# Performance work log

Measured on AMD Instinct MI355X. Metric: run time of the kernel, lower is better.

The kernel has to match this reference:

```python
import jax, jax.numpy as jnp
import numpy as np

N, E = 40000, 640000
IN_DIM, EDGE_DIM, HID = 128, 64, 128


def setup_inputs() -> dict:
    key = jax.random.key(0)
    ks = jax.random.split(key, 10)
    x = jax.random.normal(ks[0], (N, IN_DIM), dtype=jnp.float32)
    edge_index = jax.random.randint(ks[1], (2, E), 0, N, dtype=jnp.int64)
    edge_attr = jax.random.normal(ks[2], (E, EDGE_DIM), dtype=jnp.float32)
    # learned params (xavier-ish scaling)
    Wh_w = jax.random.normal(ks[3], (EDGE_DIM, HID), dtype=jnp.float32) / np.sqrt(EDGE_DIM)
    Wh_b = jnp.zeros((HID,), dtype=jnp.float32)
    Wn_w = jax.random.normal(ks[4], (2 * IN_DIM, HID), dtype=jnp.float32) / np.sqrt(2 * IN_DIM)
    Wn_b = jnp.zeros((HID,), dtype=jnp.float32)
    w_e = jax.random.normal(ks[5], (HID, 1), dtype=jnp.float32) / np.sqrt(HID)
    ft_w = jax.random.normal(ks[6], (IN_DIM, IN_DIM), dtype=jnp.float32) / np.sqrt(IN_DIM)
    ft_b = jnp.zeros((IN_DIM,), dtype=jnp.float32)
    return {"x": x, "edge_index": edge_index, "edge_attr": edge_attr,
            "Wh_w": Wh_w, "Wh_b": Wh_b, "Wn_w": Wn_w, "Wn_b": Wn_b,
            "w_e": w_e, "ft_w": ft_w, "ft_b": ft_b}


def reference(x, edge_index, edge_attr, Wh_w, Wh_b, Wn_w, Wn_b, w_e, ft_w, ft_b):
    src, dst = edge_index[0], edge_index[1]
    # gather endpoint features and run edge MLP: relu(W_h(e) + W_n([x_src; x_dst]))
    node_feat = jnp.concatenate([x[src], x[dst]], axis=1)          # [E, 2*in_dim]
    edge_h = edge_attr @ Wh_w + Wh_b                               # [E, hid]
    node_h = node_feat @ Wn_w + Wn_b                               # [E, hid]
    combined = jax.nn.relu(edge_h + node_h)
    scores = (combined @ w_e)[:, 0]                                # [E]
    alpha = jax.nn.softmax(scores, axis=0)                         # softmax over all edges
    # scatter-add weighted dst features into src nodes (same-type branch)
    local = jnp.zeros_like(x).at[src].add(-alpha[:, None] * x[dst])
    out = x + local
    out = out + out @ ft_w + ft_b
    return out
```

## Files before the change

kernel.cpp:

```cpp
#include <hip/hip_runtime.h>
#include <math.h>

#define N_NODES 40000
#define E_EDGES 640000
#define IN_DIM 128
#define EDGE_DIM 64
#define HID 128
#define EB 10000
#define NPART (EB * 4)

typedef unsigned int u32;
typedef unsigned short u16;
typedef __attribute__((ext_vector_type(4))) float f32x4;
typedef __attribute__((ext_vector_type(4))) u32 u32x4;
typedef __attribute__((ext_vector_type(8))) short bf16x8;

__device__ __forceinline__ float bf_lo(u32 d) { return __uint_as_float(d << 16); }
__device__ __forceinline__ float bf_hi(u32 d) { return __uint_as_float(d & 0xffff0000u); }
__device__ __forceinline__ u16 f2bf(float f) {
    u32 u = __float_as_uint(f);
    return (u16)((u + 0x7fffu + ((u >> 16) & 1u)) >> 16);
}
__device__ __forceinline__ u32 pack_bf(float lo, float hi) {
    return ((u32)f2bf(hi) << 16) | (u32)f2bf(lo);
}


__global__ __launch_bounds__(256) void k_pre(const float* __restrict__ x,
                                             const float* __restrict__ Whw,
                                             const float* __restrict__ Wnw,
                                             const float* __restrict__ ftw,
                                             const int* __restrict__ eidx,
                                             u16* __restrict__ xb,
                                             u32* __restrict__ counts,
                                             u16* __restrict__ Whtb,
                                             u16* __restrict__ WnAT,
                                             u16* __restrict__ WnBT,
                                             u16* __restrict__ fttb) {
    if (blockIdx.x < 20000) {
        int i = blockIdx.x * 256 + threadIdx.x;
        xb[i] = f2bf(x[i]);
    } else if (blockIdx.x < 20224) {
        int i = (blockIdx.x - 20000) * 256 + threadIdx.x;
        if (i < 8192) {
            int h = i >> 6, k = i & 63;
            Whtb[i] = f2bf(Whw[k * HID + h]);
        } else if (i < 24576) {
            int j = i - 8192, h = j >> 7, k = j & 127;
            WnAT[j] = f2bf(Wnw[k * HID + h]);
        } else if (i < 40960) {
            int j = i - 24576, h = j >> 7, k = j & 127;
            WnBT[j] = f2bf(Wnw[(IN_DIM + k) * HID + h]);
        } else {
            int j = i - 40960, h = j >> 7, k = j & 127;
            fttb[j] = f2bf(ftw[k * IN_DIM + h]);
        }
    } else {
        int e = (blockIdx.x - 20224) * 256 + threadIdx.x;
        atomicAdd(&counts[eidx[e]], 1u);
    }
}

__global__ __launch_bounds__(1024) void k_scan(const u32* __restrict__ counts,
                                               u32* __restrict__ off,
                                               u32* __restrict__ cur) {
    __shared__ u32 sums[1024];
    const int t = threadIdx.x;
    const int CH = 40;
    u32 local[CH];
    u32 s = 0;
    const int base = t * CH;
#pragma unroll
    for (int i = 0; i < CH; ++i) {
        int idx = base + i;
        u32 c = (idx < N_NODES) ? counts[idx] : 0u;
        local[i] = s;
        s += c;
    }
    sums[t] = s;
    __syncthreads();
    for (int o = 1; o < 1024; o <<= 1) {
        u32 v = (t >= o) ? sums[t - o] : 0u;
        __syncthreads();
        sums[t] += v;
        __syncthreads();
    }
    const u32 pre = sums[t] - s;
#pragma unroll
    for (int i = 0; i < CH; ++i) {
        int idx = base + i;
        if (idx < N_NODES) {
            u32 v = pre + local[i];
            off[idx] = v;
            cur[idx] = v;
        }
    }
    if (t == 1023) off[N_NODES] = sums[1023];
}

__global__ __launch_bounds__(256) void k_proj(const u16* __restrict__ xb,
                                              const u16* __restrict__ WnAT,
                                              const u16* __restrict__ WnBT,
                                              const float* __restrict__ Whb,
                                              const float* __restrict__ Wnb,
                                              u16* __restrict__ P1b,
                                              u16* __restrict__ P2b) {
    const int t = threadIdx.x, w = t >> 6, lane = t & 63;
    const int mrow = lane & 15, quad = lane >> 4;
    const int rowBase = blockIdx.x * 64 + w * 16;

    bf16x8 a[4];
    const u16* ar = xb + (size_t)(rowBase + mrow) * IN_DIM + quad * 8;
#pragma unroll
    for (int ks = 0; ks < 4; ++ks) a[ks] = *(const bf16x8*)(ar + ks * 32);

#pragma unroll
    for (int nt = 0; nt < 8; ++nt) {
        const u16* b1p = WnAT + (size_t)(nt * 16 + mrow) * IN_DIM + quad * 8;
        const u16* b2p = WnBT + (size_t)(nt * 16 + mrow) * IN_DIM + quad * 8;
        f32x4 c1 = {0.f, 0.f, 0.f, 0.f}, c2 = {0.f, 0.f, 0.f, 0.f};
#pragma unroll
        for (int ks = 0; ks < 4; ++ks) {
            c1 = __builtin_amdgcn_mfma_f32_16x16x32_bf16(a[ks], *(const bf16x8*)(b1p + ks * 32), c1, 0, 0, 0);
            c2 = __builtin_amdgcn_mfma_f32_16x16x32_bf16(a[ks], *(const bf16x8*)(b2p + ks * 32), c2, 0, 0, 0);
        }
        const int col = nt * 16 + mrow;
        const float bias = Whb[col] + Wnb[col];
#pragma unroll
        for (int r = 0; r < 4; ++r) {
            int row = rowBase + quad * 4 + r;
            P1b[(size_t)row * HID + col] = f2bf(c1[r] + bias);
            P2b[(size_t)row * HID + col] = f2bf(c2[r]);
        }
    }
}

__global__ __launch_bounds__(256) void k_edge(const int* __restrict__ eidx,
                                              const float* __restrict__ ea,
                                              const u16* __restrict__ Whtb,
                                              const u16* __restrict__ P1b,
                                              const u16* __restrict__ P2b,
                                              const float* __restrict__ we,
                                              u32* __restrict__ cur,
                                              uint2* __restrict__ sde,
                                              float* __restrict__ partials) {
    __shared__ u32 Psp[4][16][68];
    const int t = threadIdx.x, w = t >> 6, lane = t & 63;
    const int e0 = blockIdx.x * 64 + w * 16;
    const int mrow = lane & 15, quad = lane >> 4;

    const int m = lane >> 2, c4 = lane & 3;
    const int srcm = eidx[e0 + m];
    const int dstm = eidx[E_EDGES + e0 + m];
    const uint4* p1 = (const uint4*)(P1b + (size_t)srcm * HID + c4 * 32);
    const uint4* p2 = (const uint4*)(P2b + (size_t)dstm * HID + c4 * 32);
    uint4 pa[4], pb[4];
#pragma unroll
    for (int i = 0; i < 4; ++i) { pa[i] = p1[i]; pb[i] = p2[i]; }

    const f32x4* arow = (const f32x4*)(ea + (size_t)(e0 + mrow) * EDGE_DIM + quad * 8);
    f32x4 f0 = __builtin_nontemporal_load(arow);
    f32x4 f1 = __builtin_nontemporal_load(arow + 1);
    f32x4 f2 = __builtin_nontemporal_load(arow + 8);
    f32x4 f3 = __builtin_nontemporal_load(arow + 9);

#pragma unroll
    for (int i = 0; i < 4; ++i) {
        u32 da[4] = {pa[i].x, pa[i].y, pa[i].z, pa[i].w};
        u32 db[4] = {pb[i].x, pb[i].y, pb[i].z, pb[i].w};
        uint4 o;
        o.x = pack_bf(bf_lo(da[0]) + bf_lo(db[0]), bf_hi(da[0]) + bf_hi(db[0]));
        o.y = pack_bf(bf_lo(da[1]) + bf_lo(db[1]), bf_hi(da[1]) + bf_hi(db[1]));
        o.z = pack_bf(bf_lo(da[2]) + bf_lo(db[2]), bf_hi(da[2]) + bf_hi(db[2]));
        o.w = pack_bf(bf_lo(da[3]) + bf_lo(db[3]), bf_hi(da[3]) + bf_hi(db[3]));
        *(uint4*)&Psp[w][m][c4 * 16 + i * 4] = o;
    }

    bf16x8 a0, a1;
    a0[0] = (short)f2bf(f0[0]); a0[1] = (short)f2bf(f0[1]);
    a0[2] = (short)f2bf(f0[2]); a0[3] = (short)f2bf(f0[3]);
    a0[4] = (short)f2bf(f1[0]); a0[5] = (short)f2bf(f1[1]);
    a0[6] = (short)f2bf(f1[2]); a0[7] = (short)f2bf(f1[3]);
    a1[0] = (short)f2bf(f2[0]); a1[1] = (short)f2bf(f2[1]);
    a1[2] = (short)f2bf(f2[2]); a1[3] = (short)f2bf(f2[3]);
    a1[4] = (short)f2bf(f3[0]); a1[5] = (short)f2bf(f3[1]);
    a1[6] = (short)f2bf(f3[2]); a1[7] = (short)f2bf(f3[3]);

    float wsum[4] = {0.f, 0.f, 0.f, 0.f};
    const u16* bbase = Whtb + (size_t)mrow * EDGE_DIM + quad * 8;
#pragma unroll
    for (int nt = 0; nt < 8; ++nt) {
        const u16* bp = bbase + nt * 16 * EDGE_DIM;
        bf16x8 b0 = *(const bf16x8*)(bp);
        bf16x8 b1 = *(const bf16x8*)(bp + 32);
        f32x4 c = {0.f, 0.f, 0.f, 0.f};
        c = __builtin_amdgcn_mfma_f32_16x16x32_bf16(a0, b0, c, 0, 0, 0);
        c = __builtin_amdgcn_mfma_f32_16x16x32_bf16(a1, b1, c, 0, 0, 0);
        float wv = we[nt * 16 + mrow];
#pragma unroll
        for (int r = 0; r < 4; ++r) {
            u32 u = Psp[w][quad * 4 + r][nt * 8 + (mrow >> 1)];
            float p = (mrow & 1) ? bf_hi(u) : bf_lo(u);
            wsum[r] += fmaxf(c[r] + p, 0.f) * wv;
        }
    }

#pragma unroll
    for (int off = 1; off < 16; off <<= 1) {
#pragma unroll
        for (int r = 0; r < 4; ++r) wsum[r] += __shfl_xor(wsum[r], off, 16);
    }
    float ex[4]; float s4 = 0.f;
#pragma unroll
    for (int r = 0; r < 4; ++r) { ex[r] = __expf(wsum[r]); s4 += ex[r]; }

    if (mrow == 0) {
#pragma unroll
        for (int r = 0; r < 4; ++r) {
            int e = e0 + quad * 4 + r;
            int s = eidx[e];
            int d = eidx[E_EDGES + e];
            u32 pos = atomicAdd(&cur[s], 1u);
            sde[pos] = make_uint2((u32)d, __float_as_uint(-ex[r]));
        }
    }

    s4 += __shfl_xor(s4, 16, 64);
    s4 += __shfl_xor(s4, 32, 64);
    if (lane == 0) partials[blockIdx.x * 4 + w] = s4;
}

__global__ __launch_bounds__(256) void k_accum(const u32* __restrict__ off,
                                               const uint2* __restrict__ sde,
                                               const float* __restrict__ partials,
                                               float* __restrict__ sumExp,
                                               const u16* __restrict__ xb,
                                               float* __restrict__ out) {
    if (blockIdx.x == 0) {
        float s = 0.f;
        for (int i = threadIdx.x; i < NPART; i += 256) s += partials[i];
#pragma unroll
        for (int o = 1; o < 64; o <<= 1) s += __shfl_xor(s, o, 64);
        __shared__ float ws4[4];
        if ((threadIdx.x & 63) == 0) ws4[threadIdx.x >> 6] = s;
        __syncthreads();
        if (threadIdx.x == 0) sumExp[0] = ws4[0] + ws4[1] + ws4[2] + ws4[3];
        return;
    }
    const int lane = threadIdx.x & 63;
    const int n = (blockIdx.x - 1) * 4 + (threadIdx.x >> 6);
    const u32 o0 = off[n], o1 = off[n + 1];

    float acc0 = 0.f, acc1 = 0.f;
    for (u32 base = o0; base < o1; base += 64) {
        u32 j = base + (u32)lane;
        uint2 dv = make_uint2(0u, 0u);
        if (j < o1) {
            dv.x = __builtin_nontemporal_load(&sde[j].x);
            dv.y = __builtin_nontemporal_load(&sde[j].y);
        }
        int cnt = (int)min(64u, o1 - base);
        int jj = 0;
        for (; jj + 16 <= cnt; jj += 16) {
            u32 d[16]; float a[16]; u32 q[16];
#pragma unroll
            for (int k = 0; k < 16; ++k) {
                d[k] = __shfl(dv.x, jj + k, 64);
                a[k] = __uint_as_float(__shfl(dv.y, jj + k, 64));
            }
#pragma unroll
            for (int k = 0; k < 16; ++k)
                q[k] = ((const u32*)(xb + (size_t)d[k] * IN_DIM))[lane];
#pragma unroll
            for (int k = 0; k < 16; ++k) {
                acc0 = fmaf(a[k], bf_lo(q[k]), acc0);
                acc1 = fmaf(a[k], bf_hi(q[k]), acc1);
            }
        }
        for (; jj + 4 <= cnt; jj += 4) {
            u32 d[4]; float a[4]; u32 q[4];
#pragma unroll
            for (int k = 0; k < 4; ++k) {
                d[k] = __shfl(dv.x, jj + k, 64);
                a[k] = __uint_as_float(__shfl(dv.y, jj + k, 64));
            }
#pragma unroll
            for (int k = 0; k < 4; ++k)
                q[k] = ((const u32*)(xb + (size_t)d[k] * IN_DIM))[lane];
#pragma unroll
            for (int k = 0; k < 4; ++k) {
                acc0 = fmaf(a[k], bf_lo(q[k]), acc0);
                acc1 = fmaf(a[k], bf_hi(q[k]), acc1);
            }
        }
        for (; jj < cnt; ++jj) {
            u32 dst = __shfl(dv.x, jj, 64);
            float a = __uint_as_float(__shfl(dv.y, jj, 64));
            u32 q = ((const u32*)(xb + (size_t)dst * IN_DIM))[lane];
            acc0 = fmaf(a, bf_lo(q), acc0);
            acc1 = fmaf(a, bf_hi(q), acc1);
        }
    }
    float* op = out + (size_t)n * IN_DIM + 2 * lane;
    op[0] = acc0;
    op[1] = acc1;
}

__global__ __launch_bounds__(256) void k_final(const float* __restrict__ x,
                                               const u16* __restrict__ fttb,
                                               const float* __restrict__ ftb,
                                               const float* __restrict__ sumExp,
                                               float* __restrict__ out) {
    __shared__ u32 ybp[64][68];
    const float invS = 1.0f / sumExp[0];
    const int t = threadIdx.x;
    const int rb = blockIdx.x * 64;

    {
        const int rr = t >> 2, seg = t & 3;
        const float4* xp = (const float4*)(x + (size_t)(rb + rr) * IN_DIM + seg * 32);
        const float4* lp = (const float4*)(out + (size_t)(rb + rr) * IN_DIM + seg * 32);
#pragma unroll
        for (int i = 0; i < 4; ++i) {
            float4 xa = xp[2 * i], xc = xp[2 * i + 1];
            float4 la = lp[2 * i], lc = lp[2 * i + 1];
            uint4 o;
            o.x = pack_bf(fmaf(invS, la.x, xa.x), fmaf(invS, la.y, xa.y));
            o.y = pack_bf(fmaf(invS, la.z, xa.z), fmaf(invS, la.w, xa.w));
            o.z = pack_bf(fmaf(invS, lc.x, xc.x), fmaf(invS, lc.y, xc.y));
            o.w = pack_bf(fmaf(invS, lc.z, xc.z), fmaf(invS, lc.w, xc.w));
            *(uint4*)&ybp[rr][seg * 16 + i * 4] = o;
        }
    }
    __syncthreads();

    const int w = t >> 6, lane = t & 63;
    const int mrow = lane & 15, quad = lane >> 4;
    const int rowBase = rb + w * 16;

    bf16x8 a[4];
#pragma unroll
    for (int ks = 0; ks < 4; ++ks)
        a[ks] = *(const bf16x8*)&ybp[w * 16 + mrow][ks * 16 + quad * 4];

#pragma unroll
    for (int nt = 0; nt < 8; ++nt) {
        const u16* bp = fttb + (size_t)(nt * 16 + mrow) * IN_DIM + quad * 8;
        f32x4 c = {0.f, 0.f, 0.f, 0.f};
#pragma unroll
        for (int ks = 0; ks < 4; ++ks)
            c = __builtin_amdgcn_mfma_f32_16x16x32_bf16(a[ks], *(const bf16x8*)(bp + ks * 32), c, 0, 0, 0);
        const int col = nt * 16 + mrow;
        const float fb = ftb[col];
#pragma unroll
        for (int r = 0; r < 4; ++r) {
            int row = rowBase + quad * 4 + r;
            size_t idx = (size_t)row * IN_DIM + col;
            float y = fmaf(invS, out[idx], x[idx]);
            out[idx] = y + c[r] + fb;
        }
    }
}

extern "C" void kernel_launch(void* const* d_in, const int* in_sizes, int n_in,
                              void* d_out, int out_size, void* d_ws, size_t ws_size,
                              hipStream_t stream) {
    const float* x    = (const float*)d_in[0];
    const int*   eidx = (const int*)d_in[1];
    const float* ea   = (const float*)d_in[2];
    const float* Whw  = (const float*)d_in[3];
    const float* Whb  = (const float*)d_in[4];
    const float* Wnw  = (const float*)d_in[5];
    const float* Wnb  = (const float*)d_in[6];
    const float* we   = (const float*)d_in[7];
    const float* ftw  = (const float*)d_in[8];
    const float* ftb  = (const float*)d_in[9];
    float* out = (float*)d_out;

    uint2* sde      = (uint2*)d_ws;
    u16*   P1b      = (u16*)(sde + (size_t)E_EDGES);
    u16*   P2b      = P1b + (size_t)N_NODES * HID;
    u16*   xb       = P2b + (size_t)N_NODES * HID;
    u16*   Whtb     = xb + (size_t)N_NODES * IN_DIM;
    u16*   WnAT     = Whtb + (size_t)EDGE_DIM * HID;
    u16*   WnBT     = WnAT + (size_t)HID * IN_DIM;
    u16*   fttb     = WnBT + (size_t)HID * IN_DIM;
    float* partials = (float*)(fttb + (size_t)IN_DIM * IN_DIM);
    float* sumExp   = partials + NPART;
    u32*   counts   = (u32*)(sumExp + 1);
    u32*   off      = counts + N_NODES;
    u32*   cur      = off + N_NODES + 1;

    hipMemsetAsync(counts, 0, (size_t)N_NODES * sizeof(u32), stream);
    k_pre  <<<22724, 256, 0, stream>>>(x, Whw, Wnw, ftw, eidx, xb, counts,
                                       Whtb, WnAT, WnBT, fttb);
    k_scan <<<1, 1024, 0, stream>>>(counts, off, cur);
    k_proj <<<N_NODES / 64, 256, 0, stream>>>(xb, WnAT, WnBT, Whb, Wnb, P1b, P2b);
    k_edge <<<EB, 256, 0, stream>>>(eidx, ea, Whtb, P1b, P2b, we, cur, sde, partials);
    k_accum<<<N_NODES / 4 + 1, 256, 0, stream>>>(off, sde, partials, sumExp, xb, out);
    k_final<<<N_NODES / 64, 256, 0, stream>>>(x, fttb, ftb, sumExp, out);
}
```

Measured before the change: 554.0 us.

## Gather four edges per wave with 16-byte row loads in accumulation kernel

```diff
diff --git a/kernel.cpp b/kernel.cpp
--- a/kernel.cpp
+++ b/kernel.cpp
@@ -12,7 +12,6 @@
 typedef unsigned int u32;
 typedef unsigned short u16;
 typedef __attribute__((ext_vector_type(4))) float f32x4;
-typedef __attribute__((ext_vector_type(4))) u32 u32x4;
 typedef __attribute__((ext_vector_type(8))) short bf16x8;
 
 __device__ __forceinline__ float bf_lo(u32 d) { return __uint_as_float(d << 16); }
@@ -248,10 +247,12 @@
         return;
     }
     const int lane = threadIdx.x & 63;
+    const int g = lane >> 4, sub = lane & 15;
     const int n = (blockIdx.x - 1) * 4 + (threadIdx.x >> 6);
     const u32 o0 = off[n], o1 = off[n + 1];
 
-    float acc0 = 0.f, acc1 = 0.f;
+    float acc[8] = {0.f, 0.f, 0.f, 0.f, 0.f, 0.f, 0.f, 0.f};
+
     for (u32 base = o0; base < o1; base += 64) {
         u32 j = base + (u32)lane;
         uint2 dv = make_uint2(0u, 0u);
@@ -259,51 +260,42 @@
             dv.x = __builtin_nontemporal_load(&sde[j].x);
             dv.y = __builtin_nontemporal_load(&sde[j].y);
         }
-        int cnt = (int)min(64u, o1 - base);
-        int jj = 0;
-        for (; jj + 16 <= cnt; jj += 16) {
-            u32 d[16]; float a[16]; u32 q[16];
-#pragma unroll
-            for (int k = 0; k < 16; ++k) {
-                d[k] = __shfl(dv.x, jj + k, 64);
-                a[k] = __uint_as_float(__shfl(dv.y, jj + k, 64));
+        const int cnt = (int)min(64u, o1 - base);
+        for (int jj = 0; jj < cnt; jj += 16) {
+            float av[4]; uint4 q[4];
+#pragma unroll
+            for (int b = 0; b < 4; ++b) {
+                int sl = jj + b * 4 + g;
+                u32 dr = __shfl(dv.x, sl, 64);
+                av[b] = __uint_as_float(__shfl(dv.y, sl, 64));
+                q[b] = ((const uint4*)(xb + (size_t)dr * IN_DIM))[sub];
             }
 #pragma unroll
-            for (int k = 0; k < 16; ++k)
-                q[k] = ((const u32*)(xb + (size_t)d[k] * IN_DIM))[lane];
-#pragma unroll
-            for (int k = 0; k < 16; ++k) {
-                acc0 = fmaf(a[k], bf_lo(q[k]), acc0);
-                acc1 = fmaf(a[k], bf_hi(q[k]), acc1);
+            for (int b = 0; b < 4; ++b) {
+                acc[0] = fmaf(av[b], bf_lo(q[b].x), acc[0]);
+                acc[1] = fmaf(av[b], bf_hi(q[b].x), acc[1]);
+                acc[2] = fmaf(av[b], bf_lo(q[b].y), acc[2]);
+                acc[3] = fmaf(av[b], bf_hi(q[b].y), acc[3]);
+                acc[4] = fmaf(av[b], bf_lo(q[b].z), acc[4]);
+                acc[5] = fmaf(av[b], bf_hi(q[b].z), acc[5]);
+                acc[6] = fmaf(av[b], bf_lo(q[b].w), acc[6]);
+                acc[7] = fmaf(av[b], bf_hi(q[b].w), acc[7]);
             }
         }
-        for (; jj + 4 <= cnt; jj += 4) {
-            u32 d[4]; float a[4]; u32 q[4];
-#pragma unroll
-            for (int k = 0; k < 4; ++k) {
-                d[k] = __shfl(dv.x, jj + k, 64);
-                a[k] = __uint_as_float(__shfl(dv.y, jj + k, 64));
-            }
-#pragma unroll
-            for (int k = 0; k < 4; ++k)
-                q[k] = ((const u32*)(xb + (size_t)d[k] * IN_DIM))[lane];
-#pragma unroll
-            for (int k = 0; k < 4; ++k) {
-                acc0 = fmaf(a[k], bf_lo(q[k]), acc0);
-                acc1 = fmaf(a[k], bf_hi(q[k]), acc1);
-            }
-        }
-        for (; jj < cnt; ++jj) {
-            u32 dst = __shfl(dv.x, jj, 64);
-            float a = __uint_as_float(__shfl(dv.y, jj, 64));
-            u32 q = ((const u32*)(xb + (size_t)dst * IN_DIM))[lane];
-            acc0 = fmaf(a, bf_lo(q), acc0);
-            acc1 = fmaf(a, bf_hi(q), acc1);
-        }
-    }
-    float* op = out + (size_t)n * IN_DIM + 2 * lane;
-    op[0] = acc0;
-    op[1] = acc1;
+    }
+
+#pragma unroll
+    for (int k = 0; k < 8; ++k) {
+        acc[k] += __shfl_xor(acc[k], 16, 64);
+        acc[k] += __shfl_xor(acc[k], 32, 64);
+    }
+    if (g == 0) {
+        float* op = out + (size_t)n * IN_DIM + sub * 8;
+        float4 v0 = make_float4(acc[0], acc[1], acc[2], acc[3]);
+        float4 v1 = make_float4(acc[4], acc[5], acc[6], acc[7]);
+        *(float4*)op = v0;
+        *(float4*)(op + 4) = v1;
+    }
 }
 
 __global__ __launch_bounds__(256) void k_final(const float* __restrict__ x,
```

New measurement: 558.5 us. Within noise of the previous version (+0.8%).
